# Kernel tuning notes

Measured on AMD Instinct MI355X. Metric: run time of the kernel, lower is better.

## Reference

```python
import jax, jax.numpy as jnp
import numpy as np

B, T, D, H = 4, 2048, 1024, 16
DH = D // H  # 64


def setup_inputs() -> dict:
    key = jax.random.key(0)
    ks = jax.random.split(key, 5)
    s = 0.02
    return {
        "x": jax.random.normal(ks[0], (B, T, D), dtype=jnp.float32),
        "Wq": jax.random.normal(ks[1], (D, D), dtype=jnp.float32) * s,
        "Wk": jax.random.normal(ks[2], (D, D), dtype=jnp.float32) * s,
        "Wv": jax.random.normal(ks[3], (D, D), dtype=jnp.float32) * s,
        "Wo": jax.random.normal(ks[4], (D, D), dtype=jnp.float32) * s,
        "bo": jnp.zeros((D,), dtype=jnp.float32),
    }


def reference(x, Wq, Wk, Wv, Wo, bo):
    b, t, d = x.shape
    # QKV projections (no bias, matching qkv_bias=False)
    q = (x @ Wq).reshape(b, t, H, DH).transpose(0, 2, 1, 3)  # [B,H,T,Dh]
    k = (x @ Wk).reshape(b, t, H, DH).transpose(0, 2, 1, 3)
    v = (x @ Wv).reshape(b, t, H, DH).transpose(0, 2, 1, 3)
    scores = jnp.einsum('bhqd,bhkd->bhqk', q, k)  # [B,H,T,T]
    # mask strictly-upper triangle (future positions) with -inf, then scale
    causal = jnp.triu(jnp.ones((t, t), dtype=bool), k=1)
    scores = jnp.where(causal[None, None], -jnp.inf, scores)
    attn = jax.nn.softmax(scores / np.float32(np.sqrt(DH)), axis=-1)
    ctx = jnp.einsum('bhqk,bhkd->bhqd', attn, v)  # [B,H,T,Dh]
    ctx = ctx.transpose(0, 2, 1, 3).reshape(b, t, d)
    return ctx @ Wo + bo
```

## Files before the change

kernel.cpp:

```cpp
#include <hip/hip_runtime.h>
#include <math.h>
#include <stdint.h>

typedef unsigned short u16;
typedef __bf16 bf16x8 __attribute__((ext_vector_type(8)));
typedef unsigned short u16x8 __attribute__((ext_vector_type(8)));
typedef float f32x4 __attribute__((ext_vector_type(4)));

constexpr int Tc = 2048, Dc = 1024, Hc = 16, Mc = 8192;
constexpr size_t NQKV = (size_t)Mc * Dc;
constexpr size_t NW = (size_t)Dc * Dc;

__device__ __forceinline__ u16 f2bf(float f) {
    union { float f; uint32_t u; } c; c.f = f;
    uint32_t u = c.u;
    u += 0x7FFFu + ((u >> 16) & 1u);
    return (u16)(u >> 16);
}

__device__ __forceinline__ bf16x8 ldbf8(const u16* p) {
    u16x8 v = *(const u16x8*)p;
    return __builtin_bit_cast(bf16x8, v);
}

__device__ __forceinline__ float fexp2(float x) {
#if __has_builtin(__builtin_amdgcn_exp2f)
    return __builtin_amdgcn_exp2f(x);
#else
    return exp2f(x);
#endif
}

__device__ __forceinline__ void gload_lds16(const void* g, void* l) {
    __builtin_amdgcn_global_load_lds(
        (__attribute__((address_space(1))) void*)(uintptr_t)g,
        (__attribute__((address_space(3))) void*)l, 16, 0, 0);
}

__global__ __launch_bounds__(256)
void cvt_x_kernel(const float* __restrict__ x, u16* __restrict__ xb)
{
    int i = blockIdx.x * 256 + threadIdx.x;
    float4 v = ((const float4*)x)[i];
    ushort4 o;
    o.x = f2bf(v.x); o.y = f2bf(v.y); o.z = f2bf(v.z); o.w = f2bf(v.w);
    ((ushort4*)xb)[i] = o;
}

__global__ __launch_bounds__(256)
void wt_cvt_kernel(const float* __restrict__ Wq, const float* __restrict__ Wk,
                   const float* __restrict__ Wv, const float* __restrict__ Wo,
                   u16* __restrict__ WTq, u16* __restrict__ WTk,
                   u16* __restrict__ WTv, u16* __restrict__ WTo)
{
    __shared__ float Ts[64][65];
    const int z = blockIdx.z;
    const float* W = (z == 0) ? Wq : (z == 1) ? Wk : (z == 2) ? Wv : Wo;
    u16* WT        = (z == 0) ? WTq : (z == 1) ? WTk : (z == 2) ? WTv : WTo;
    const int k0 = blockIdx.x * 64, n0 = blockIdx.y * 64;
    const int tid = threadIdx.x;
    #pragma unroll
    for (int it = 0; it < 16; ++it) {
        int flat = it * 256 + tid;
        int r = flat >> 6, c = flat & 63;
        Ts[r][c] = W[(size_t)(k0 + r) * Dc + n0 + c];
    }
    __syncthreads();
    #pragma unroll
    for (int it = 0; it < 16; ++it) {
        int flat = it * 256 + tid;
        int rn = flat >> 6, ck = flat & 63;
        WT[(size_t)(n0 + rn) * Dc + k0 + ck] = f2bf(Ts[ck][rn]);
    }
}

__global__ __launch_bounds__(256)
void qkv_gemm_kernel(const u16* __restrict__ xb,
                     const u16* __restrict__ WTq, const u16* __restrict__ WTk,
                     const u16* __restrict__ WTv,
                     u16* __restrict__ Qb, u16* __restrict__ Kb, u16* __restrict__ Vb)
{
    const int z = blockIdx.z;
    const u16* WT = (z == 0) ? WTq : (z == 1) ? WTk : WTv;
    u16* outp     = (z == 0) ? Qb  : (z == 1) ? Kb  : Vb;
    const float scale = (z == 0) ? 0.125f * 1.44269504088896f : 1.0f;

    __shared__ __align__(16) u16 As[128 * 32];
    __shared__ __align__(16) u16 Bs[128 * 32];

    const int tid = threadIdx.x, lane = tid & 63, w = tid >> 6;
    const int wm = w >> 1, wn = w & 1;
    const int m0 = blockIdx.x * 128, n0 = blockIdx.y * 128;

    f32x4 acc[4][4] = {};

    for (int k0 = 0; k0 < Dc; k0 += 32) {
        __syncthreads();
        #pragma unroll
        for (int t = 0; t < 2; ++t) {
            int ci = w * 64 + t * 256 + lane;
            int r = ci >> 2, p = ci & 3;
            int pc = p ^ ((r >> 1) & 3);
            gload_lds16(xb + (size_t)(m0 + r) * Dc + k0 + pc * 8,
                        As + (size_t)(w * 64 + t * 256) * 8);
            gload_lds16(WT + (size_t)(n0 + r) * Dc + k0 + pc * 8,
                        Bs + (size_t)(w * 64 + t * 256) * 8);
        }
        __syncthreads();

        bf16x8 a[4], b[4];
        #pragma unroll
        for (int i = 0; i < 4; ++i) {
            int row = wm * 64 + i * 16 + (lane & 15);
            a[i] = ldbf8(As + row * 32 + (((lane >> 4) ^ ((row >> 1) & 3)) * 8));
            int col = wn * 64 + i * 16 + (lane & 15);
            b[i] = ldbf8(Bs + col * 32 + (((lane >> 4) ^ ((col >> 1) & 3)) * 8));
        }
        #pragma unroll
        for (int i = 0; i < 4; ++i)
            #pragma unroll
            for (int j = 0; j < 4; ++j)
                acc[i][j] = __builtin_amdgcn_mfma_f32_16x16x32_bf16(a[i], b[j], acc[i][j], 0, 0, 0);
    }

    #pragma unroll
    for (int j = 0; j < 4; ++j) {
        int n = n0 + wn * 64 + j * 16 + (lane & 15);
        int hh = n >> 6, dh = n & 63;
        #pragma unroll
        for (int i = 0; i < 4; ++i) {
            #pragma unroll
            for (int r = 0; r < 4; ++r) {
                int m = m0 + wm * 64 + i * 16 + (lane >> 4) * 4 + r;
                int bb = m >> 11, t = m & 2047;
                outp[((size_t)(bb * Hc + hh) * Tc + t) * 64 + dh] = f2bf(acc[i][j][r] * scale);
            }
        }
    }
}

__global__ __launch_bounds__(256)
void v_transpose_kernel(const u16* __restrict__ Vb, u16* __restrict__ VTb)
{
    __shared__ u16 Ts[64][68];
    const int tid = threadIdx.x;
    const int bh = blockIdx.y, t0 = blockIdx.x * 64;
    const size_t vbase = (size_t)bh * Tc * 64;
    #pragma unroll
    for (int it = 0; it < 4; ++it) {
        int flat = it * 1024 + tid * 4;
        int r = flat >> 6, c = flat & 63;
        *(ushort4*)&Ts[r][c] = *(const ushort4*)(Vb + vbase + (size_t)(t0 + r) * 64 + c);
    }
    __syncthreads();
    const size_t obase = (size_t)bh * 64 * Tc;
    #pragma unroll
    for (int it = 0; it < 4; ++it) {
        int flat = it * 1024 + tid * 4;
        int d = flat >> 6, tl = flat & 63;
        ushort4 o;
        o.x = Ts[tl][d]; o.y = Ts[tl + 1][d]; o.z = Ts[tl + 2][d]; o.w = Ts[tl + 3][d];
        *(ushort4*)(VTb + obase + (size_t)d * Tc + t0 + tl) = o;
    }
}

__global__ __launch_bounds__(256)
void attn_mfma_kernel(const u16* __restrict__ Qb, const u16* __restrict__ Kb,
                      const u16* __restrict__ VTb, u16* __restrict__ ctxb)
{
    __shared__ __align__(16) u16 Ks[64 * 64];
    __shared__ __align__(16) u16 Vs[64 * 64];
    __shared__ __align__(16) u16 Ps[4][32 * 72];

    const int tid = threadIdx.x, lane = tid & 63, w = tid >> 6;
    const int g = lane >> 4, lq = lane & 15;
    const int id = blockIdx.x;
    const int xcd = id & 7, j = id >> 3;
    const int bh = (xcd << 3) | (j & 7);
    const int qt = 15 - (j >> 3);
    const size_t qkbase = (size_t)bh * Tc * 64;
    const size_t vtbase = (size_t)bh * 64 * Tc;
    const int b = bh >> 4, h = bh & 15;
    u16* pw = &Ps[w][0];

    const int q0 = qt * 128;
    const int nkt = qt * 2 + 2;

    bf16x8 qf[2][2];
    #pragma unroll
    for (int qfi = 0; qfi < 2; ++qfi)
        #pragma unroll
        for (int kf = 0; kf < 2; ++kf) {
            int row = q0 + w * 32 + qfi * 16 + lq;
            qf[qfi][kf] = ldbf8(Qb + qkbase + (size_t)row * 64 + kf * 32 + g * 8);
        }

    f32x4 o_acc[2][4] = {};
    float m_run[2] = {-INFINITY, -INFINITY};
    float l_run[2] = {0.f, 0.f};

    for (int kt = 0; kt < nkt; ++kt) {
        const int kv0 = kt * 64;
        __syncthreads();
        #pragma unroll
        for (int t = 0; t < 2; ++t) {
            int ci = w * 64 + t * 256 + lane;
            int r = ci >> 3, p = ci & 7;
            int pc = p ^ (r & 7);
            gload_lds16(Kb + qkbase + (size_t)(kv0 + r) * 64 + pc * 8,
                        Ks + (size_t)(w * 64 + t * 256) * 8);
            gload_lds16(VTb + vtbase + (size_t)r * Tc + kv0 + pc * 8,
                        Vs + (size_t)(w * 64 + t * 256) * 8);
        }
        __syncthreads();

        f32x4 s[4][2] = {};
        __builtin_amdgcn_s_setprio(1);
        #pragma unroll
        for (int kf = 0; kf < 2; ++kf) {
            bf16x8 kb[4];
            #pragma unroll
            for (int ni = 0; ni < 4; ++ni) {
                int rr = ni * 16 + lq;
                int pc = (g + 4 * kf) ^ (rr & 7);
                kb[ni] = ldbf8(Ks + rr * 64 + pc * 8);
            }
            #pragma unroll
            for (int ni = 0; ni < 4; ++ni)
                #pragma unroll
                for (int qfi = 0; qfi < 2; ++qfi)
                    s[ni][qfi] = __builtin_amdgcn_mfma_f32_16x16x32_bf16(kb[ni], qf[qfi][kf], s[ni][qfi], 0, 0, 0);
        }
        __builtin_amdgcn_s_setprio(0);

        if (kt >= nkt - 2) {
            #pragma unroll
            for (int ni = 0; ni < 4; ++ni)
                #pragma unroll
                for (int qfi = 0; qfi < 2; ++qfi)
                    #pragma unroll
                    for (int r = 0; r < 4; ++r) {
                        int kv = kv0 + ni * 16 + 4 * g + r;
                        int q  = q0 + w * 32 + qfi * 16 + lq;
                        if (kv > q) s[ni][qfi][r] = -INFINITY;
                    }
        }

        #pragma unroll
        for (int qfi = 0; qfi < 2; ++qfi) {
            float mrow = -INFINITY;
            #pragma unroll
            for (int ni = 0; ni < 4; ++ni)
                #pragma unroll
                for (int r = 0; r < 4; ++r) mrow = fmaxf(mrow, s[ni][qfi][r]);
            mrow = fmaxf(mrow, __shfl_xor(mrow, 16, 64));
            mrow = fmaxf(mrow, __shfl_xor(mrow, 32, 64));
            if (!__all(mrow <= m_run[qfi] + 12.0f)) {
                float mnew  = fmaxf(m_run[qfi], mrow);
                float alpha = fexp2(m_run[qfi] - mnew);
                m_run[qfi] = mnew;
                l_run[qfi] *= alpha;
                #pragma unroll
                for (int r = 0; r < 4; ++r) {
                    float ar = __shfl(alpha, 4 * g + r, 16);
                    #pragma unroll
                    for (int nd = 0; nd < 4; ++nd) o_acc[qfi][nd][r] *= ar;
                }
            }
            float mq = m_run[qfi];
            float sum = 0.f;
            #pragma unroll
            for (int ni = 0; ni < 4; ++ni)
                #pragma unroll
                for (int r = 0; r < 4; ++r) {
                    float pe = fexp2(s[ni][qfi][r] - mq);
                    s[ni][qfi][r] = pe;
                    sum += pe;
                }
            sum += __shfl_xor(sum, 16, 64);
            sum += __shfl_xor(sum, 32, 64);
            l_run[qfi] += sum;
        }

        #pragma unroll
        for (int qfi = 0; qfi < 2; ++qfi)
            #pragma unroll
            for (int ni = 0; ni < 4; ++ni) {
                float a0 = s[ni][qfi][0], a1 = s[ni][qfi][1];
                float a2 = s[ni][qfi][2], a3 = s[ni][qfi][3];
                uint32_t lo, hi;
                asm volatile("v_cvt_pk_bf16_f32 %0, %1, %2" : "=v"(lo) : "v"(a0), "v"(a1));
                asm volatile("v_cvt_pk_bf16_f32 %0, %1, %2" : "=v"(hi) : "v"(a2), "v"(a3));
                uint2 pk = make_uint2(lo, hi);
                *(uint2*)(pw + (qfi * 16 + lq) * 72 + ni * 16 + 4 * g) = pk;
            }

        bf16x8 pa[2][2];
        #pragma unroll
        for (int qfi = 0; qfi < 2; ++qfi)
            #pragma unroll
            for (int kf = 0; kf < 2; ++kf)
                pa[qfi][kf] = ldbf8(pw + (qfi * 16 + lq) * 72 + kf * 32 + 8 * g);
        __builtin_amdgcn_s_setprio(1);
        #pragma unroll
        for (int kf = 0; kf < 2; ++kf) {
            bf16x8 vb[4];
            #pragma unroll
            for (int nd = 0; nd < 4; ++nd) {
                int rr = nd * 16 + lq;
                int pc = (g + 4 * kf) ^ (rr & 7);
                vb[nd] = ldbf8(Vs + rr * 64 + pc * 8);
            }
            #pragma unroll
            for (int qfi = 0; qfi < 2; ++qfi)
                #pragma unroll
                for (int nd = 0; nd < 4; ++nd)
                    o_acc[qfi][nd] = __builtin_amdgcn_mfma_f32_16x16x32_bf16(pa[qfi][kf], vb[nd], o_acc[qfi][nd], 0, 0, 0);
        }
        __builtin_amdgcn_s_setprio(0);
    }

    #pragma unroll
    for (int qfi = 0; qfi < 2; ++qfi)
        #pragma unroll
        for (int r = 0; r < 4; ++r) {
            float lr = __shfl(l_run[qfi], 4 * g + r, 16);
            float inv = 1.0f / lr;
            int qrow = q0 + w * 32 + qfi * 16 + 4 * g + r;
            #pragma unroll
            for (int nd = 0; nd < 4; ++nd) {
                int d = h * 64 + nd * 16 + lq;
                ctxb[(size_t)(b * Tc + qrow) * Dc + d] = f2bf(o_acc[qfi][nd][r] * inv);
            }
        }
}

__global__ __launch_bounds__(256)
void out_gemm_kernel(const u16* __restrict__ ctxb, const u16* __restrict__ WTo,
                     const float* __restrict__ bo, float* __restrict__ out)
{
    __shared__ __align__(16) u16 As[128 * 32];
    __shared__ __align__(16) u16 Bs[128 * 32];

    const int tid = threadIdx.x, lane = tid & 63, w = tid >> 6;
    const int wm = w >> 1, wn = w & 1;
    const int m0 = blockIdx.x * 128, n0 = blockIdx.y * 128;

    f32x4 acc[4][4] = {};

    for (int k0 = 0; k0 < Dc; k0 += 32) {
        __syncthreads();
        #pragma unroll
        for (int t = 0; t < 2; ++t) {
            int ci = w * 64 + t * 256 + lane;
            int r = ci >> 2, p = ci & 3;
            int pc = p ^ ((r >> 1) & 3);
            gload_lds16(ctxb + (size_t)(m0 + r) * Dc + k0 + pc * 8,
                        As + (size_t)(w * 64 + t * 256) * 8);
            gload_lds16(WTo + (size_t)(n0 + r) * Dc + k0 + pc * 8,
                        Bs + (size_t)(w * 64 + t * 256) * 8);
        }
        __syncthreads();

        bf16x8 a[4], b[4];
        #pragma unroll
        for (int i = 0; i < 4; ++i) {
            int row = wm * 64 + i * 16 + (lane & 15);
            a[i] = ldbf8(As + row * 32 + (((lane >> 4) ^ ((row >> 1) & 3)) * 8));
            int col = wn * 64 + i * 16 + (lane & 15);
            b[i] = ldbf8(Bs + col * 32 + (((lane >> 4) ^ ((col >> 1) & 3)) * 8));
        }
        #pragma unroll
        for (int i = 0; i < 4; ++i)
            #pragma unroll
            for (int j = 0; j < 4; ++j)
                acc[i][j] = __builtin_amdgcn_mfma_f32_16x16x32_bf16(a[i], b[j], acc[i][j], 0, 0, 0);
    }

    #pragma unroll
    for (int j = 0; j < 4; ++j) {
        int n = n0 + wn * 64 + j * 16 + (lane & 15);
        float bias = bo[n];
        #pragma unroll
        for (int i = 0; i < 4; ++i) {
            #pragma unroll
            for (int r = 0; r < 4; ++r) {
                int m = m0 + wm * 64 + i * 16 + (lane >> 4) * 4 + r;
                out[(size_t)m * Dc + n] = acc[i][j][r] + bias;
            }
        }
    }
}

extern "C" void kernel_launch(void* const* d_in, const int* in_sizes, int n_in,
                              void* d_out, int out_size, void* d_ws, size_t ws_size,
                              hipStream_t stream)
{
    const float* x  = (const float*)d_in[0];
    const float* Wq = (const float*)d_in[1];
    const float* Wk = (const float*)d_in[2];
    const float* Wv = (const float*)d_in[3];
    const float* Wo = (const float*)d_in[4];
    const float* bo = (const float*)d_in[5];
    float* out = (float*)d_out;

    u16* xb   = (u16*)d_ws;
    u16* WTq  = xb + NQKV;
    u16* WTk  = WTq + NW;
    u16* WTv  = WTk + NW;
    u16* WTo  = WTv + NW;
    u16* Qb   = WTo + NW;
    u16* Kb   = Qb + NQKV;
    u16* Vb   = Kb + NQKV;
    u16* VTb  = Vb + NQKV;
    u16* ctxb = VTb + NQKV;

    cvt_x_kernel<<<8192, 256, 0, stream>>>(x, xb);
    wt_cvt_kernel<<<dim3(16, 16, 4), 256, 0, stream>>>(Wq, Wk, Wv, Wo, WTq, WTk, WTv, WTo);
    qkv_gemm_kernel<<<dim3(64, 8, 3), 256, 0, stream>>>(xb, WTq, WTk, WTv, Qb, Kb, Vb);
    v_transpose_kernel<<<dim3(32, 64), 256, 0, stream>>>(Vb, VTb);
    attn_mfma_kernel<<<dim3(1024), 256, 0, stream>>>(Qb, Kb, VTb, ctxb);
    out_gemm_kernel<<<dim3(64, 8), 256, 0, stream>>>(ctxb, WTo, bo, out);
}
```

Before: 254.5 us.

## Double-buffer K/V tiles in attention kernel to overlap loads with MFMA

Splits the shared K and V tiles into two buffers. The first tile is loaded before the loop, and inside the loop the next tile's global-to-LDS loads are issued before the current tile is computed on. This hides global-load latency behind the QK and PV MFMA work and cuts the barriers per iteration from two to one. In exchange, K/V shared memory per block doubles, which may lower the number of blocks resident per CU.

New measurement: 258.9 us. About the same (+1.7%).

```diff
diff --git a/kernel.cpp b/kernel.cpp
--- a/kernel.cpp
+++ b/kernel.cpp
@@ -168,8 +168,8 @@
 void attn_mfma_kernel(const u16* __restrict__ Qb, const u16* __restrict__ Kb,
                       const u16* __restrict__ VTb, u16* __restrict__ ctxb)
 {
-    __shared__ __align__(16) u16 Ks[64 * 64];
-    __shared__ __align__(16) u16 Vs[64 * 64];
+    __shared__ __align__(16) u16 Ks[2][64 * 64];
+    __shared__ __align__(16) u16 Vs[2][64 * 64];
     __shared__ __align__(16) u16 Ps[4][32 * 72];
 
     const int tid = threadIdx.x, lane = tid & 63, w = tid >> 6;
@@ -199,20 +199,37 @@
     float m_run[2] = {-INFINITY, -INFINITY};
     float l_run[2] = {0.f, 0.f};
 
+    #pragma unroll
+    for (int t = 0; t < 2; ++t) {
+        int ci = w * 64 + t * 256 + lane;
+        int r = ci >> 3, p = ci & 7;
+        int pc = p ^ (r & 7);
+        gload_lds16(Kb + qkbase + (size_t)r * 64 + pc * 8,
+                    &Ks[0][0] + (size_t)(w * 64 + t * 256) * 8);
+        gload_lds16(VTb + vtbase + (size_t)r * Tc + pc * 8,
+                    &Vs[0][0] + (size_t)(w * 64 + t * 256) * 8);
+    }
+    __syncthreads();
+
+    int cur = 0;
     for (int kt = 0; kt < nkt; ++kt) {
+        if (kt + 1 < nkt) {
+            const int kv1 = (kt + 1) * 64;
+            #pragma unroll
+            for (int t = 0; t < 2; ++t) {
+                int ci = w * 64 + t * 256 + lane;
+                int r = ci >> 3, p = ci & 7;
+                int pc = p ^ (r & 7);
+                gload_lds16(Kb + qkbase + (size_t)(kv1 + r) * 64 + pc * 8,
+                            &Ks[cur ^ 1][0] + (size_t)(w * 64 + t * 256) * 8);
+                gload_lds16(VTb + vtbase + (size_t)r * Tc + kv1 + pc * 8,
+                            &Vs[cur ^ 1][0] + (size_t)(w * 64 + t * 256) * 8);
+            }
+        }
+
         const int kv0 = kt * 64;
-        __syncthreads();
-        #pragma unroll
-        for (int t = 0; t < 2; ++t) {
-            int ci = w * 64 + t * 256 + lane;
-            int r = ci >> 3, p = ci & 7;
-            int pc = p ^ (r & 7);
-            gload_lds16(Kb + qkbase + (size_t)(kv0 + r) * 64 + pc * 8,
-                        Ks + (size_t)(w * 64 + t * 256) * 8);
-            gload_lds16(VTb + vtbase + (size_t)r * Tc + kv0 + pc * 8,
-                        Vs + (size_t)(w * 64 + t * 256) * 8);
-        }
-        __syncthreads();
+        const u16* ks = &Ks[cur][0];
+        const u16* vs = &Vs[cur][0];
 
         f32x4 s[4][2] = {};
         __builtin_amdgcn_s_setprio(1);
@@ -223,7 +240,7 @@
             for (int ni = 0; ni < 4; ++ni) {
                 int rr = ni * 16 + lq;
                 int pc = (g + 4 * kf) ^ (rr & 7);
-                kb[ni] = ldbf8(Ks + rr * 64 + pc * 8);
+                kb[ni] = ldbf8(ks + rr * 64 + pc * 8);
             }
             #pragma unroll
             for (int ni = 0; ni < 4; ++ni)
@@ -309,7 +326,7 @@
             for (int nd = 0; nd < 4; ++nd) {
                 int rr = nd * 16 + lq;
                 int pc = (g + 4 * kf) ^ (rr & 7);
-                vb[nd] = ldbf8(Vs + rr * 64 + pc * 8);
+                vb[nd] = ldbf8(vs + rr * 64 + pc * 8);
             }
             #pragma unroll
             for (int qfi = 0; qfi < 2; ++qfi)
@@ -318,6 +335,9 @@
                     o_acc[qfi][nd] = __builtin_amdgcn_mfma_f32_16x16x32_bf16(pa[qfi][kf], vb[nd], o_acc[qfi][nd], 0, 0, 0);
         }
         __builtin_amdgcn_s_setprio(0);
+
+        if (kt + 1 < nkt) __syncthreads();
+        cur ^= 1;
     }
 
     #pragma unroll
```
